# Kernel optimization log

Hardware: AMD Instinct MI355X
Metric: run time of the kernel (lower is better)

The kernel has to match this reference:

```python
import jax, jax.numpy as jnp
import numpy as np

H = 12          # num attention heads
D_HEAD = 64     # head size (768 / 12)
P = 2           # power-law exponent
C = 5.0         # score shift
EPS = 1e-10


def setup_inputs() -> dict:
    key = jax.random.key(0)
    ks = jax.random.split(key, 8)
    B, S, Dm = 32, 512, 768
    scale = 1.0 / np.sqrt(Dm)
    return {
        "hidden_states": jax.random.normal(ks[0], (B, S, Dm), dtype=jnp.float32),
        "attention_mask": jnp.ones((B, 1, 1, S), dtype=jnp.float32),
        "Wq": jax.random.normal(ks[1], (Dm, Dm), dtype=jnp.float32) * scale,
        "bq": jnp.zeros((Dm,), dtype=jnp.float32),
        "Wk": jax.random.normal(ks[2], (Dm, Dm), dtype=jnp.float32) * scale,
        "bk": jnp.zeros((Dm,), dtype=jnp.float32),
        "Wv": jax.random.normal(ks[3], (Dm, Dm), dtype=jnp.float32) * scale,
        "bv": jnp.zeros((Dm,), dtype=jnp.float32),
    }


def _heads(x, B, S):
    # [B, S, H*d] -> [B, H, S, d]
    return x.reshape(B, S, H, D_HEAD).transpose(0, 2, 1, 3)


def reference(hidden_states, attention_mask, Wq, bq, Wk, bk, Wv, bv):
    B, S, Dm = hidden_states.shape
    q = _heads(hidden_states @ Wq + bq, B, S)
    k = _heads(hidden_states @ Wk + bk, B, S)
    v = _heads(hidden_states @ Wv + bv, B, S)

    inv_sqrt_d = 1.0 / (np.sqrt(D_HEAD) + 1e-10)
    scores = jnp.einsum("bhqd,bhkd->bhqk", q, k) * inv_sqrt_d  # [B,H,S,S]

    # Power-law attention (Powerformer, distill=0 branch)
    probs = jnp.power(scores + C, P)
    probs = probs / (jnp.sum(probs, axis=-1, keepdims=True) + EPS)
    probs = probs * attention_mask  # mask multiplied after normalization

    ctx = jnp.einsum("bhqk,bhkd->bhqd", probs, v)  # [B,H,S,d]
    ctx = ctx.transpose(0, 2, 1, 3).reshape(B, S, Dm)
    return ctx
```

## Files before the change

### kernel.cpp

```cpp
#include <hip/hip_runtime.h>

typedef __attribute__((ext_vector_type(8))) _Float16 half8;
typedef __attribute__((ext_vector_type(4))) _Float16 half4;
typedef __attribute__((ext_vector_type(4))) float f32x4;

#define MFMA_K32(a, b, c) __builtin_amdgcn_mfma_f32_16x16x32_f16((a), (b), (c), 0, 0, 0)
#define MFMA_K16(a, b, c) __builtin_amdgcn_mfma_f32_16x16x16f16((a), (b), (c), 0, 0, 0)

__device__ inline void async16(const _Float16* g, _Float16* l) {
    __builtin_amdgcn_global_load_lds(
        (const __attribute__((address_space(1))) void*)g,
        (__attribute__((address_space(3))) void*)l, 16, 0, 0);
}


__global__ __launch_bounds__(256) void xcast(const float* __restrict__ X,
                                             _Float16* __restrict__ Xh)
{
    size_t idx = ((size_t)blockIdx.x * 256 + threadIdx.x) * 8;
    float4 a = *(const float4*)(X + idx);
    float4 c = *(const float4*)(X + idx + 4);
    half8 hv;
    hv[0] = (_Float16)a.x; hv[1] = (_Float16)a.y;
    hv[2] = (_Float16)a.z; hv[3] = (_Float16)a.w;
    hv[4] = (_Float16)c.x; hv[5] = (_Float16)c.y;
    hv[6] = (_Float16)c.z; hv[7] = (_Float16)c.w;
    *(half8*)(Xh + idx) = hv;
}

__global__ __launch_bounds__(256) void wcast_kernel(
    const float* __restrict__ W0, const float* __restrict__ W1,
    const float* __restrict__ W2,
    _Float16* __restrict__ T0, _Float16* __restrict__ T1,
    _Float16* __restrict__ T2)
{
    int z = blockIdx.z;
    const float* W = (z == 0) ? W0 : (z == 1) ? W1 : W2;
    _Float16* T = (z == 0) ? T0 : (z == 1) ? T1 : T2;
    __shared__ float tile[32][33];
    int n0 = blockIdx.x * 32, k0 = blockIdx.y * 32;
    int tx = threadIdx.x & 31, ty = threadIdx.x >> 5;
#pragma unroll
    for (int r = 0; r < 4; ++r)
        tile[ty + 8 * r][tx] = W[(size_t)(k0 + ty + 8 * r) * 768 + n0 + tx];
    __syncthreads();
#pragma unroll
    for (int r = 0; r < 4; ++r)
        T[(size_t)(n0 + ty + 8 * r) * 768 + k0 + tx] =
            (_Float16)tile[tx][ty + 8 * r];
}

__global__ __launch_bounds__(256) void qkv_gemm(
    const _Float16* __restrict__ Xh,
    const _Float16* __restrict__ W0, const _Float16* __restrict__ W1,
    const _Float16* __restrict__ W2,
    const float* __restrict__ b0, const float* __restrict__ b1,
    const float* __restrict__ b2,
    const float* __restrict__ mask,
    _Float16* __restrict__ Qo, _Float16* __restrict__ Ko,
    _Float16* __restrict__ Vo)
{
    int z = blockIdx.y / 6;
    int n0 = (blockIdx.y % 6) * 128;
    int m0 = blockIdx.x * 128;
    const _Float16* Wt = (z == 0) ? W0 : (z == 1) ? W1 : W2;
    const float* bias = (z == 0) ? b0 : (z == 1) ? b1 : b2;

    __shared__ __attribute__((aligned(16))) _Float16 As[128 * 32];
    __shared__ __attribute__((aligned(16))) _Float16 Bs[128 * 32];

    int t = threadIdx.x;
    int wave = t >> 6, lane = t & 63, quad = lane >> 4, l16 = lane & 15;
    int wm = (wave & 1) * 64, wn = (wave >> 1) * 64;

    int srow0 = t >> 2;
    int sblk = (t & 3) ^ ((srow0 >> 1) & 3);

    const _Float16* ga0 = Xh + (size_t)(m0 + srow0) * 768 + sblk * 8;
    const _Float16* ga1 = Xh + (size_t)(m0 + 64 + srow0) * 768 + sblk * 8;
    const _Float16* gb0 = Wt + (size_t)(n0 + srow0) * 768 + sblk * 8;
    const _Float16* gb1 = Wt + (size_t)(n0 + 64 + srow0) * 768 + sblk * 8;
    _Float16* la0 = As + wave * 512;
    _Float16* la1 = As + 2048 + wave * 512;
    _Float16* lb0 = Bs + wave * 512;
    _Float16* lb1 = Bs + 2048 + wave * 512;

    int swz = ((quad ^ ((l16 >> 1) & 3)) << 3);

    f32x4 acc[4][4] = {};

    for (int k0 = 0; k0 < 768; k0 += 32) {
        async16(ga0, la0); async16(ga1, la1);
        async16(gb0, lb0); async16(gb1, lb1);
        ga0 += 32; ga1 += 32; gb0 += 32; gb1 += 32;
        __syncthreads();
        half8 af[4], bf[4];
#pragma unroll
        for (int i = 0; i < 4; ++i)
            af[i] = *(const half8*)&As[(wm + i * 16 + l16) * 32 + swz];
#pragma unroll
        for (int j = 0; j < 4; ++j)
            bf[j] = *(const half8*)&Bs[(wn + j * 16 + l16) * 32 + swz];
#pragma unroll
        for (int i = 0; i < 4; ++i)
#pragma unroll
            for (int j = 0; j < 4; ++j)
                acc[i][j] = MFMA_K32(af[i], bf[j], acc[i][j]);
        __syncthreads();
    }

    float mk[4][4];
    if (z == 2) {
#pragma unroll
        for (int i = 0; i < 4; ++i) {
            int mbase = m0 + wm + i * 16 + quad * 4;
            int bb = mbase >> 9, s = mbase & 511;
#pragma unroll
            for (int r = 0; r < 4; ++r)
                mk[i][r] = mask[(size_t)bb * 512 + s + r];
        }
    }
#pragma unroll
    for (int j = 0; j < 4; ++j) {
        int n = n0 + wn + j * 16 + l16;
        float bv = bias[n];
        int hh = n >> 6, d = n & 63;
#pragma unroll
        for (int i = 0; i < 4; ++i) {
            int mbase = m0 + wm + i * 16 + quad * 4;
            int bb = mbase >> 9, s = mbase & 511;
            if (z < 2) {
                _Float16* outp = (z == 0) ? Qo : Ko;
#pragma unroll
                for (int r = 0; r < 4; ++r) {
                    size_t off = (((size_t)(bb * 12 + hh)) * 512 + s + r) * 64 + d;
                    outp[off] = (_Float16)(acc[i][j][r] + bv);
                }
            } else {
                half4 pk;
#pragma unroll
                for (int r = 0; r < 4; ++r)
                    pk[r] = (_Float16)((acc[i][j][r] + bv) * mk[i][r]);
                size_t off = (((size_t)(bb * 12 + hh)) * 64 + d) * 512 + s;
                *(half4*)&Vo[off] = pk;
            }
        }
    }
}

__global__ __launch_bounds__(128) void attn_kernel(
    const _Float16* __restrict__ Q, const _Float16* __restrict__ K,
    const _Float16* __restrict__ Vt, float* __restrict__ out)
{
    __shared__ __attribute__((aligned(16))) _Float16 Ks[64 * 88];
    __shared__ __attribute__((aligned(16))) _Float16 Vs[64 * 88];

    int t = threadIdx.x;
    int wave = t >> 6, lane = t & 63, quad = lane >> 4, l16 = lane & 15;
    int h = blockIdx.y, b = blockIdx.z;
    size_t bh = (size_t)b * 12 + h;
    const _Float16* Qp = Q + bh * (512 * 64);
    const _Float16* Kp = K + bh * (512 * 64);
    const _Float16* Vp = Vt + bh * (64 * 512);
    int qbase = blockIdx.x * 128 + wave * 64;

    half8 qf[4][2];
#pragma unroll
    for (int i = 0; i < 4; ++i)
#pragma unroll
        for (int ks = 0; ks < 2; ++ks)
            qf[i][ks] = *(const half8*)(Qp + (size_t)(qbase + i * 16 + l16) * 64 +
                                        ks * 32 + quad * 8);

    f32x4 ctx[4][4] = {};
    f32x4 rsum[4] = {};
    const half4 ones = {(_Float16)1.f, (_Float16)1.f, (_Float16)1.f, (_Float16)1.f};

    int srow = t >> 1, spart = (t & 1) * 32;

    for (int kt = 0; kt < 8; ++kt) {
        int k0 = kt * 64;
        const _Float16* kg = Kp + (size_t)(k0 + srow) * 64 + spart;
        half8 ka0 = *(const half8*)kg;
        half8 ka1 = *(const half8*)(kg + 8);
        half8 ka2 = *(const half8*)(kg + 16);
        half8 ka3 = *(const half8*)(kg + 24);
        const _Float16* vg = Vp + (size_t)srow * 512 + k0 + spart;
        half8 va0 = *(const half8*)vg;
        half8 va1 = *(const half8*)(vg + 8);
        half8 va2 = *(const half8*)(vg + 16);
        half8 va3 = *(const half8*)(vg + 24);
        __syncthreads();
        *(half8*)&Ks[srow * 88 + spart] = ka0;
        *(half8*)&Ks[srow * 88 + spart + 8] = ka1;
        *(half8*)&Ks[srow * 88 + spart + 16] = ka2;
        *(half8*)&Ks[srow * 88 + spart + 24] = ka3;
        *(half8*)&Vs[srow * 88 + spart] = va0;
        *(half8*)&Vs[srow * 88 + spart + 8] = va1;
        *(half8*)&Vs[srow * 88 + spart + 16] = va2;
        *(half8*)&Vs[srow * 88 + spart + 24] = va3;
        __syncthreads();

#pragma unroll
        for (int kb = 0; kb < 4; ++kb) {
            half8 kf0 = *(const half8*)&Ks[(kb * 16 + l16) * 88 + quad * 8];
            half8 kf1 = *(const half8*)&Ks[(kb * 16 + l16) * 88 + 32 + quad * 8];
            half4 pA[4];
#pragma unroll
            for (int i = 0; i < 4; ++i) {
                f32x4 sc = {0.f, 0.f, 0.f, 0.f};
                sc = MFMA_K32(kf0, qf[i][0], sc);
                sc = MFMA_K32(kf1, qf[i][1], sc);
                half4 p;
#pragma unroll
                for (int r = 0; r < 4; ++r) {
                    float s = sc[r] * 0.125f + 5.0f;
                    p[r] = (_Float16)(s * s);
                }
                pA[i] = p;
                rsum[i] = MFMA_K16(p, ones, rsum[i]);
            }
#pragma unroll
            for (int n = 0; n < 4; ++n) {
                half4 vf = *(const half4*)&Vs[(n * 16 + l16) * 88 + kb * 16 + quad * 4];
#pragma unroll
                for (int i = 0; i < 4; ++i)
                    ctx[i][n] = MFMA_K16(pA[i], vf, ctx[i][n]);
            }
        }
    }

#pragma unroll
    for (int i = 0; i < 4; ++i) {
        f32x4 inv;
#pragma unroll
        for (int r = 0; r < 4; ++r)
            inv[r] = 1.0f / (rsum[i][r] + 1e-10f);
#pragma unroll
        for (int n = 0; n < 4; ++n)
#pragma unroll
            for (int r = 0; r < 4; ++r) {
                int q = qbase + i * 16 + quad * 4 + r;
                int d = n * 16 + l16;
                out[((size_t)b * 512 + q) * 768 + h * 64 + d] =
                    ctx[i][n][r] * inv[r];
            }
    }
}

extern "C" void kernel_launch(void* const* d_in, const int* in_sizes, int n_in,
                              void* d_out, int out_size, void* d_ws, size_t ws_size,
                              hipStream_t stream)
{
    const float* hs   = (const float*)d_in[0];
    const float* mask = (const float*)d_in[1];
    const float* Wq   = (const float*)d_in[2];
    const float* bq   = (const float*)d_in[3];
    const float* Wk   = (const float*)d_in[4];
    const float* bk   = (const float*)d_in[5];
    const float* Wv   = (const float*)d_in[6];
    const float* bv   = (const float*)d_in[7];
    float* out = (float*)d_out;

    char* ws = (char*)d_ws;
    _Float16* Wtq = (_Float16*)ws;
    _Float16* Wtk = Wtq + 768 * 768;
    _Float16* Wtv = Wtk + 768 * 768;
    _Float16* Qb  = Wtv + 768 * 768;
    _Float16* Kb  = Qb + 16384 * 768;
    _Float16* Vb  = Kb + 16384 * 768;
    _Float16* Xh = (_Float16*)d_out;

    xcast<<<dim3(6144), 256, 0, stream>>>(hs, Xh);
    wcast_kernel<<<dim3(24, 24, 3), 256, 0, stream>>>(Wq, Wk, Wv, Wtq, Wtk, Wtv);
    qkv_gemm<<<dim3(128, 18), 256, 0, stream>>>(Xh, Wtq, Wtk, Wtv,
                                                bq, bk, bv, mask, Qb, Kb, Vb);
    attn_kernel<<<dim3(4, 12, 32), 128, 0, stream>>>(Qb, Kb, Vb, out);
}
```

Measured before the change: 267.1 us.

## Deepen GEMM K-tile to 64, fold score scale into Q, widen attention blocks

The QKV GEMM now stages a 64-wide K slice per iteration with an XOR swizzle across 8 chunks, which halves the number of barrier pairs per block. The 1/sqrt(d) scale is folded into Q when it is written out, so the attention inner loop saves one multiply per score. The attention kernel now runs 256 threads covering 256 queries per block, so each K/V tile loaded into shared memory is reused by four waves instead of two. The trade-off is twice the shared memory per GEMM block, which may lower occupancy. Pre-scaling Q also slightly changes fp16 rounding.

```diff
diff --git a/kernel.cpp b/kernel.cpp
--- a/kernel.cpp
+++ b/kernel.cpp
@@ -66,46 +66,51 @@
     const _Float16* Wt = (z == 0) ? W0 : (z == 1) ? W1 : W2;
     const float* bias = (z == 0) ? b0 : (z == 1) ? b1 : b2;
 
-    __shared__ __attribute__((aligned(16))) _Float16 As[128 * 32];
-    __shared__ __attribute__((aligned(16))) _Float16 Bs[128 * 32];
+    __shared__ __attribute__((aligned(16))) _Float16 As[128 * 64];
+    __shared__ __attribute__((aligned(16))) _Float16 Bs[128 * 64];
 
     int t = threadIdx.x;
     int wave = t >> 6, lane = t & 63, quad = lane >> 4, l16 = lane & 15;
     int wm = (wave & 1) * 64, wn = (wave >> 1) * 64;
 
-    int srow0 = t >> 2;
-    int sblk = (t & 3) ^ ((srow0 >> 1) & 3);
-
-    const _Float16* ga0 = Xh + (size_t)(m0 + srow0) * 768 + sblk * 8;
-    const _Float16* ga1 = Xh + (size_t)(m0 + 64 + srow0) * 768 + sblk * 8;
-    const _Float16* gb0 = Wt + (size_t)(n0 + srow0) * 768 + sblk * 8;
-    const _Float16* gb1 = Wt + (size_t)(n0 + 64 + srow0) * 768 + sblk * 8;
-    _Float16* la0 = As + wave * 512;
-    _Float16* la1 = As + 2048 + wave * 512;
-    _Float16* lb0 = Bs + wave * 512;
-    _Float16* lb1 = Bs + 2048 + wave * 512;
-
-    int swz = ((quad ^ ((l16 >> 1) & 3)) << 3);
+    int srow = t >> 3;
+    int sg = (t & 7) ^ (srow & 7);
+
+    const _Float16* gA = Xh + (size_t)(m0 + srow) * 768 + sg * 8;
+    const _Float16* gB = Wt + (size_t)(n0 + srow) * 768 + sg * 8;
+    _Float16* lA = As + t * 8;
+    _Float16* lB = Bs + t * 8;
 
     f32x4 acc[4][4] = {};
 
-    for (int k0 = 0; k0 < 768; k0 += 32) {
-        async16(ga0, la0); async16(ga1, la1);
-        async16(gb0, lb0); async16(gb1, lb1);
-        ga0 += 32; ga1 += 32; gb0 += 32; gb1 += 32;
-        __syncthreads();
-        half8 af[4], bf[4];
-#pragma unroll
-        for (int i = 0; i < 4; ++i)
-            af[i] = *(const half8*)&As[(wm + i * 16 + l16) * 32 + swz];
-#pragma unroll
-        for (int j = 0; j < 4; ++j)
-            bf[j] = *(const half8*)&Bs[(wn + j * 16 + l16) * 32 + swz];
-#pragma unroll
-        for (int i = 0; i < 4; ++i)
-#pragma unroll
-            for (int j = 0; j < 4; ++j)
-                acc[i][j] = MFMA_K32(af[i], bf[j], acc[i][j]);
+    for (int k0 = 0; k0 < 768; k0 += 64) {
+#pragma unroll
+        for (int q = 0; q < 4; ++q) {
+            async16(gA + (size_t)q * 32 * 768 + k0, lA + q * 2048);
+            async16(gB + (size_t)q * 32 * 768 + k0, lB + q * 2048);
+        }
+        __syncthreads();
+#pragma unroll
+        for (int ks = 0; ks < 2; ++ks) {
+            half8 af[4], bf[4];
+#pragma unroll
+            for (int i = 0; i < 4; ++i) {
+                int row = wm + i * 16 + l16;
+                af[i] = *(const half8*)&As[row * 64 +
+                                           (((ks << 2) + quad) ^ (row & 7)) * 8];
+            }
+#pragma unroll
+            for (int j = 0; j < 4; ++j) {
+                int row = wn + j * 16 + l16;
+                bf[j] = *(const half8*)&Bs[row * 64 +
+                                           (((ks << 2) + quad) ^ (row & 7)) * 8];
+            }
+#pragma unroll
+            for (int i = 0; i < 4; ++i)
+#pragma unroll
+                for (int j = 0; j < 4; ++j)
+                    acc[i][j] = MFMA_K32(af[i], bf[j], acc[i][j]);
+        }
         __syncthreads();
     }
 
@@ -129,12 +134,17 @@
         for (int i = 0; i < 4; ++i) {
             int mbase = m0 + wm + i * 16 + quad * 4;
             int bb = mbase >> 9, s = mbase & 511;
-            if (z < 2) {
-                _Float16* outp = (z == 0) ? Qo : Ko;
+            if (z == 0) {
 #pragma unroll
                 for (int r = 0; r < 4; ++r) {
                     size_t off = (((size_t)(bb * 12 + hh)) * 512 + s + r) * 64 + d;
-                    outp[off] = (_Float16)(acc[i][j][r] + bv);
+                    Qo[off] = (_Float16)((acc[i][j][r] + bv) * 0.125f);
+                }
+            } else if (z == 1) {
+#pragma unroll
+                for (int r = 0; r < 4; ++r) {
+                    size_t off = (((size_t)(bb * 12 + hh)) * 512 + s + r) * 64 + d;
+                    Ko[off] = (_Float16)(acc[i][j][r] + bv);
                 }
             } else {
                 half4 pk;
@@ -148,7 +158,7 @@
     }
 }
 
-__global__ __launch_bounds__(128) void attn_kernel(
+__global__ __launch_bounds__(256) void attn_kernel(
     const _Float16* __restrict__ Q, const _Float16* __restrict__ K,
     const _Float16* __restrict__ Vt, float* __restrict__ out)
 {
@@ -162,7 +172,7 @@
     const _Float16* Qp = Q + bh * (512 * 64);
     const _Float16* Kp = K + bh * (512 * 64);
     const _Float16* Vp = Vt + bh * (64 * 512);
-    int qbase = blockIdx.x * 128 + wave * 64;
+    int qbase = blockIdx.x * 256 + wave * 64;
 
     half8 qf[4][2];
 #pragma unroll
@@ -176,29 +186,21 @@
     f32x4 rsum[4] = {};
     const half4 ones = {(_Float16)1.f, (_Float16)1.f, (_Float16)1.f, (_Float16)1.f};
 
-    int srow = t >> 1, spart = (t & 1) * 32;
+    int srow = t >> 2, spart = (t & 3) * 16;
 
     for (int kt = 0; kt < 8; ++kt) {
         int k0 = kt * 64;
         const _Float16* kg = Kp + (size_t)(k0 + srow) * 64 + spart;
         half8 ka0 = *(const half8*)kg;
         half8 ka1 = *(const half8*)(kg + 8);
-        half8 ka2 = *(const half8*)(kg + 16);
-        half8 ka3 = *(const half8*)(kg + 24);
         const _Float16* vg = Vp + (size_t)srow * 512 + k0 + spart;
         half8 va0 = *(const half8*)vg;
         half8 va1 = *(const half8*)(vg + 8);
-        half8 va2 = *(const half8*)(vg + 16);
-        half8 va3 = *(const half8*)(vg + 24);
         __syncthreads();
         *(half8*)&Ks[srow * 88 + spart] = ka0;
         *(half8*)&Ks[srow * 88 + spart + 8] = ka1;
-        *(half8*)&Ks[srow * 88 + spart + 16] = ka2;
-        *(half8*)&Ks[srow * 88 + spart + 24] = ka3;
         *(half8*)&Vs[srow * 88 + spart] = va0;
         *(half8*)&Vs[srow * 88 + spart + 8] = va1;
-        *(half8*)&Vs[srow * 88 + spart + 16] = va2;
-        *(half8*)&Vs[srow * 88 + spart + 24] = va3;
         __syncthreads();
 
 #pragma unroll
@@ -214,7 +216,7 @@
                 half4 p;
 #pragma unroll
                 for (int r = 0; r < 4; ++r) {
-                    float s = sc[r] * 0.125f + 5.0f;
+                    float s = sc[r] + 5.0f;
                     p[r] = (_Float16)(s * s);
                 }
                 pA[i] = p;
@@ -275,5 +277,5 @@
     wcast_kernel<<<dim3(24, 24, 3), 256, 0, stream>>>(Wq, Wk, Wv, Wtq, Wtk, Wtv);
     qkv_gemm<<<dim3(128, 18), 256, 0, stream>>>(Xh, Wtq, Wtk, Wtv,
                                                 bq, bk, bv, mask, Qb, Kb, Vb);
-    attn_kernel<<<dim3(4, 12, 32), 128, 0, stream>>>(Qb, Kb, Vb, out);
-}
+    attn_kernel<<<dim3(2, 12, 32), 256, 0, stream>>>(Qb, Kb, Vb, out);
+}
```

Result: faster. 241.3 us (-9.7%).
